# Kernel tuning notes

Measured on AMD Instinct MI355X. Metric: run time of the kernel, lower is better.

Reference implementation:

```python
import jax, jax.numpy as jnp
import numpy as np

B, T, C = 4, 4096, 1024
NH, DH = 16, 128          # n_head, d_head = d_qkv // n_head
DQKV, DR = 2048, 256      # d_qkv, d_rank


def _uniform(key, shape, bound):
    return jax.random.uniform(key, shape, jnp.float32, -bound, bound)


def setup_inputs() -> dict:
    key = jax.random.key(0)
    k0, k1, k2, k3, k4 = jax.random.split(key, 5)
    # CastedLinear init: bound = sqrt(3) * 0.5 * in_features**-0.5 (same for w1, w2)
    b_qkv = (3 ** 0.5) * 0.5 * C ** (-0.5)
    b_proj = (3 ** 0.5) * 0.5 * DQKV ** (-0.5)
    return {
        "x": jax.random.normal(k0, (B, T, C), jnp.float32),
        "qkv_w1": _uniform(k1, (DR, C), b_qkv),
        "qkv_w2": _uniform(k2, (3 * DQKV, DR), b_qkv),
        "cproj_w1": _uniform(k3, (DR, DQKV), b_proj),
        "cproj_w2": _uniform(k4, (2 * C, DR), b_proj),
    }


def _rmsnorm(x):
    eps = jnp.finfo(x.dtype).eps  # F.rms_norm default eps
    return x * jax.lax.rsqrt(jnp.mean(x * x, axis=-1, keepdims=True) + eps)


def reference(x, qkv_w1, qkv_w2, cproj_w1, cproj_w2):
    Bx, Tx, Cx = x.shape
    # qkv projection with low-rank factorization + relu^2 activation between factors
    h = _rmsnorm(x) @ qkv_w1.T                      # [B,T,DR]
    h = jnp.square(jax.nn.relu(h))
    qkv = (h @ qkv_w2.T).reshape(Bx, Tx, 3 * NH, DH)
    q, k, v = jnp.split(qkv, 3, axis=2)             # each [B,T,NH,DH]
    q, k = _rmsnorm(q), _rmsnorm(k)

    # rotary embedding: half the head dim rotated, second quarter frequencies zero
    quarter = DH // 4
    freq = (1.0 / 1024.0) ** jnp.linspace(0.0, 1.0, quarter)
    freq = jnp.concatenate([freq, jnp.zeros(quarter, freq.dtype)])  # [DH//2]
    theta = jnp.arange(Tx, dtype=jnp.float32)[:, None] * freq[None, :]
    cos = jnp.cos(theta)[None, :, None, :]          # [1,T,1,DH//2]
    sin = jnp.sin(theta)[None, :, None, :]

    def rope(z):
        z1, z2 = jnp.split(z, 2, axis=-1)
        return jnp.concatenate([z1 * cos + z2 * sin, -z1 * sin + z2 * cos], axis=-1)

    q, k = rope(q), rope(k)

    # causal linear attention: sigmoid-gated cumulative sum over time
    y = jax.nn.relu(q) * jnp.cumsum(jax.nn.sigmoid(k) * v, axis=1)  # [B,T,NH,DH]
    y = y.reshape(Bx, Tx, NH * DH)

    # low-rank output projection (no activation), gated residual
    uv = (y @ cproj_w1.T) @ cproj_w2.T              # [B,T,2C]
    u, g = jnp.split(uv, 2, axis=-1)
    return x + u * jax.nn.silu(g)
```

## Files before the change

kernel.cpp:

```cpp
#include <hip/hip_runtime.h>
#include <hip/hip_bf16.h>

#define TB 4
#define TT 4096
#define TC 1024
#define TNH 16
#define TDH 128
#define TDQKV 2048
#define TDR 256
#define RB 4096
#define ROWS (TB*TT)
#define SLAB (RB*128)

typedef __attribute__((ext_vector_type(8))) short bfx8;
typedef __attribute__((ext_vector_type(4))) float fx4;
typedef __attribute__((address_space(1))) const unsigned char GAS;
typedef __attribute__((address_space(3))) unsigned char LAS;

__device__ __forceinline__ unsigned short f2b(float f) {
    unsigned int u = __float_as_uint(f);
    unsigned int r = (u + 0x7fffu + ((u >> 16) & 1u)) >> 16;
    return (unsigned short)r;
}
__device__ __forceinline__ float b2f(unsigned short h) {
    return __uint_as_float(((unsigned int)h) << 16);
}
__device__ __forceinline__ float sigm(float x) {
    return 1.0f / (1.0f + __expf(-x));
}
__device__ __forceinline__ int xcd_swz(int hw, int nwg) {
    int q = nwg >> 3;
    return (hw & 7) * q + (hw >> 3);
}

__global__ __launch_bounds__(256) void cvt_bf16(const float* __restrict__ in,
                                                unsigned short* __restrict__ out, int n) {
    int i = (blockIdx.x * 256 + threadIdx.x) * 4;
    if (i < n) {
        float4 v = *(const float4*)(in + i);
        out[i + 0] = f2b(v.x);
        out[i + 1] = f2b(v.y);
        out[i + 2] = f2b(v.z);
        out[i + 3] = f2b(v.w);
    }
}

__global__ __launch_bounds__(256) void rope_tab(float* __restrict__ ct, float* __restrict__ st) {
    int i = blockIdx.x * 256 + threadIdx.x;
    int t = i >> 5, j = i & 31;
    float fr = exp2f(-10.0f * (float)j / 31.0f);
    float th = (float)t * fr;
    ct[i] = cosf(th);
    st[i] = sinf(th);
}

__global__ __launch_bounds__(256) void rmsnorm_x(const float* __restrict__ x,
                                                 unsigned short* __restrict__ xn) {
    int row = blockIdx.x;
    int tid = threadIdx.x;
    float4 v = *(const float4*)(x + (size_t)row * TC + tid * 4);
    float ss = v.x * v.x + v.y * v.y + v.z * v.z + v.w * v.w;
    #pragma unroll
    for (int o = 32; o > 0; o >>= 1) ss += __shfl_xor(ss, o);
    __shared__ float red[4];
    if ((tid & 63) == 0) red[tid >> 6] = ss;
    __syncthreads();
    float tot = red[0] + red[1] + red[2] + red[3];
    float sc = rsqrtf(tot * (1.0f / TC) + 1.1920929e-7f);
    unsigned short* o = xn + (size_t)row * TC + tid * 4;
    o[0] = f2b(v.x * sc); o[1] = f2b(v.y * sc); o[2] = f2b(v.z * sc); o[3] = f2b(v.w * sc);
}

template <int EPI>
__global__ __launch_bounds__(256) void gemm_bt(const unsigned short* __restrict__ A, int lda,
                                               const unsigned short* __restrict__ Bm,
                                               unsigned short* __restrict__ C, int ldc,
                                               int N, int K) {
    __shared__ unsigned short As[2][128 * 32];
    __shared__ unsigned short Bs[2][128 * 32];
    const int m0 = blockIdx.y * 128;
    const int n0 = blockIdx.x * 128;
    const int tid = threadIdx.x;
    const int lane = tid & 63;
    const int w = tid >> 6;
    const int wr = w >> 1, wc = w & 1;
    const int r16 = lane & 15;
    const int kk = (lane >> 4) * 8;
    const int l4 = lane >> 2;
    const int c8 = (lane & 3) * 8;
    const int nk = K >> 5;
    fx4 acc[4][4] = {};

    auto stage = [&](int buf, int k0) {
        #pragma unroll
        for (int i = 0; i < 2; ++i) {
            int rr = (w + 4 * i) * 16 + l4;
            const unsigned short* ga = A + (size_t)(m0 + rr) * lda + k0 + c8;
            const unsigned short* gb = Bm + (size_t)(n0 + rr) * K + k0 + c8;
            __builtin_amdgcn_global_load_lds((GAS*)ga, (LAS*)&As[buf][(w + 4 * i) * 512], 16, 0, 0);
            __builtin_amdgcn_global_load_lds((GAS*)gb, (LAS*)&Bs[buf][(w + 4 * i) * 512], 16, 0, 0);
        }
    };

    stage(0, 0);
    __syncthreads();
    int buf = 0;
    for (int ks = 0; ks < nk; ++ks) {
        if (ks + 1 < nk) stage(buf ^ 1, (ks + 1) * 32);
        bfx8 af[4], bfr[4];
        #pragma unroll
        for (int mi = 0; mi < 4; mi++) af[mi] = *(const bfx8*)&As[buf][(wr * 64 + mi * 16 + r16) * 32 + kk];
        #pragma unroll
        for (int ni = 0; ni < 4; ni++) bfr[ni] = *(const bfx8*)&Bs[buf][(wc * 64 + ni * 16 + r16) * 32 + kk];
        #pragma unroll
        for (int mi = 0; mi < 4; mi++)
            #pragma unroll
            for (int ni = 0; ni < 4; ni++)
                acc[mi][ni] = __builtin_amdgcn_mfma_f32_16x16x32_bf16(af[mi], bfr[ni], acc[mi][ni], 0, 0, 0);
        __syncthreads();
        buf ^= 1;
    }

    const int rg = lane >> 4;
    #pragma unroll
    for (int mi = 0; mi < 4; mi++)
        #pragma unroll
        for (int ni = 0; ni < 4; ni++) {
            int col = n0 + wc * 64 + ni * 16 + r16;
            #pragma unroll
            for (int r = 0; r < 4; r++) {
                int row = m0 + wr * 64 + mi * 16 + rg * 4 + r;
                float v = acc[mi][ni][r];
                if (EPI == 1) { v = fmaxf(v, 0.0f); v *= v; }
                if (EPI == 2) {
                    int head = col >> 7;
                    C[(size_t)head * SLAB + (size_t)row * 128 + (col & 127)] = f2b(v);
                } else {
                    C[(size_t)row * ldc + col] = f2b(v);
                }
            }
        }
}

template <int EPI, int NX>
__global__ __launch_bounds__(256) void gemm_bt64(const unsigned short* __restrict__ A, int lda,
                                                 const unsigned short* __restrict__ Bm,
                                                 unsigned short* __restrict__ C, int ldc,
                                                 int K) {
    __shared__ unsigned short As[2][64 * 32];
    __shared__ unsigned short Bs[2][64 * 32];
    const int hw = blockIdx.y * gridDim.x + blockIdx.x;
    const int lg = xcd_swz(hw, gridDim.x * gridDim.y);
    const int n0 = (lg % NX) * 64;
    const int m0 = (lg / NX) * 64;
    const int tid = threadIdx.x;
    const int lane = tid & 63;
    const int w = tid >> 6;
    const int wr = w >> 1, wc = w & 1;
    const int r16 = lane & 15;
    const int kk = (lane >> 4) * 8;
    const int l4 = lane >> 2;
    const int c8 = (lane & 3) * 8;
    const int nk = K >> 5;
    fx4 acc[2][2] = {};

    auto stage = [&](int buf, int k0) {
        int rr = w * 16 + l4;
        const unsigned short* ga = A + (size_t)(m0 + rr) * lda + k0 + c8;
        const unsigned short* gb = Bm + (size_t)(n0 + rr) * K + k0 + c8;
        __builtin_amdgcn_global_load_lds((GAS*)ga, (LAS*)&As[buf][w * 512], 16, 0, 0);
        __builtin_amdgcn_global_load_lds((GAS*)gb, (LAS*)&Bs[buf][w * 512], 16, 0, 0);
    };

    stage(0, 0);
    __syncthreads();
    int buf = 0;
    for (int ks = 0; ks < nk; ++ks) {
        if (ks + 1 < nk) stage(buf ^ 1, (ks + 1) * 32);
        bfx8 af[2], bfr[2];
        #pragma unroll
        for (int mi = 0; mi < 2; mi++) af[mi] = *(const bfx8*)&As[buf][(wr * 32 + mi * 16 + r16) * 32 + kk];
        #pragma unroll
        for (int ni = 0; ni < 2; ni++) bfr[ni] = *(const bfx8*)&Bs[buf][(wc * 32 + ni * 16 + r16) * 32 + kk];
        #pragma unroll
        for (int mi = 0; mi < 2; mi++)
            #pragma unroll
            for (int ni = 0; ni < 2; ni++)
                acc[mi][ni] = __builtin_amdgcn_mfma_f32_16x16x32_bf16(af[mi], bfr[ni], acc[mi][ni], 0, 0, 0);
        __syncthreads();
        buf ^= 1;
    }

    const int rg = lane >> 4;
    #pragma unroll
    for (int mi = 0; mi < 2; mi++)
        #pragma unroll
        for (int ni = 0; ni < 2; ni++) {
            int col = n0 + wc * 32 + ni * 16 + r16;
            #pragma unroll
            for (int r = 0; r < 4; r++) {
                int row = m0 + wr * 32 + mi * 16 + rg * 4 + r;
                float v = acc[mi][ni][r];
                if (EPI == 1) { v = fmaxf(v, 0.0f); v *= v; }
                C[(size_t)row * ldc + col] = f2b(v);
            }
        }
}

__global__ __launch_bounds__(256, 2) void gemm4f(const unsigned short* __restrict__ A,
                                                 const unsigned short* __restrict__ Wm,
                                                 const float* __restrict__ x,
                                                 float* __restrict__ out) {
    __shared__ unsigned short As[2][128 * 32];
    __shared__ unsigned short Bu[2][128 * 32];
    __shared__ unsigned short Bg[2][128 * 32];
    const int hw = blockIdx.y * gridDim.x + blockIdx.x;
    const int lg = xcd_swz(hw, gridDim.x * gridDim.y);
    const int n0 = (lg & 7) * 128;
    const int m0 = (lg >> 3) * 128;
    const int tid = threadIdx.x;
    const int lane = tid & 63;
    const int w = tid >> 6;
    const int wr = w >> 1, wc = w & 1;
    const int r16 = lane & 15;
    const int kk = (lane >> 4) * 8;
    const int l4 = lane >> 2;
    const int c8 = (lane & 3) * 8;
    fx4 accu[4][4] = {};
    fx4 accg[4][4] = {};

    auto stage = [&](int buf, int k0) {
        #pragma unroll
        for (int i = 0; i < 2; ++i) {
            int rr = (w + 4 * i) * 16 + l4;
            const unsigned short* ga = A + (size_t)(m0 + rr) * TDR + k0 + c8;
            const unsigned short* gu = Wm + (size_t)(n0 + rr) * TDR + k0 + c8;
            const unsigned short* gg = Wm + (size_t)(1024 + n0 + rr) * TDR + k0 + c8;
            __builtin_amdgcn_global_load_lds((GAS*)ga, (LAS*)&As[buf][(w + 4 * i) * 512], 16, 0, 0);
            __builtin_amdgcn_global_load_lds((GAS*)gu, (LAS*)&Bu[buf][(w + 4 * i) * 512], 16, 0, 0);
            __builtin_amdgcn_global_load_lds((GAS*)gg, (LAS*)&Bg[buf][(w + 4 * i) * 512], 16, 0, 0);
        }
    };

    stage(0, 0);
    __syncthreads();
    int buf = 0;
    for (int ks = 0; ks < 8; ++ks) {
        if (ks + 1 < 8) stage(buf ^ 1, (ks + 1) * 32);
        bfx8 af[4], bu[4], bg[4];
        #pragma unroll
        for (int mi = 0; mi < 4; mi++) af[mi] = *(const bfx8*)&As[buf][(wr * 64 + mi * 16 + r16) * 32 + kk];
        #pragma unroll
        for (int ni = 0; ni < 4; ni++) {
            bu[ni] = *(const bfx8*)&Bu[buf][(wc * 64 + ni * 16 + r16) * 32 + kk];
            bg[ni] = *(const bfx8*)&Bg[buf][(wc * 64 + ni * 16 + r16) * 32 + kk];
        }
        #pragma unroll
        for (int mi = 0; mi < 4; mi++)
            #pragma unroll
            for (int ni = 0; ni < 4; ni++) {
                accu[mi][ni] = __builtin_amdgcn_mfma_f32_16x16x32_bf16(af[mi], bu[ni], accu[mi][ni], 0, 0, 0);
                accg[mi][ni] = __builtin_amdgcn_mfma_f32_16x16x32_bf16(af[mi], bg[ni], accg[mi][ni], 0, 0, 0);
            }
        __syncthreads();
        buf ^= 1;
    }

    const int rg = lane >> 4;
    #pragma unroll
    for (int mi = 0; mi < 4; mi++)
        #pragma unroll
        for (int ni = 0; ni < 4; ni++) {
            int col = n0 + wc * 64 + ni * 16 + r16;
            #pragma unroll
            for (int r = 0; r < 4; r++) {
                int row = m0 + wr * 64 + mi * 16 + rg * 4 + r;
                float u = accu[mi][ni][r];
                float g = accg[mi][ni][r];
                size_t idx = (size_t)row * TC + col;
                out[idx] = x[idx] + u * (g * sigm(g));
            }
        }
}

__global__ __launch_bounds__(256) void qk_post(unsigned short* __restrict__ qkv,
                                               const float* __restrict__ ct,
                                               const float* __restrict__ st) {
    int gri = blockIdx.x * 4 + (threadIdx.x >> 6);
    int lane = threadIdx.x & 63;
    int h32 = gri >> 12;
    int t = gri & (RB - 1);
    size_t base = (size_t)h32 * SLAB + (size_t)t * 128;
    float e0 = b2f(qkv[base + lane]);
    float e1 = b2f(qkv[base + 64 + lane]);
    float ss = e0 * e0 + e1 * e1;
    #pragma unroll
    for (int o = 32; o > 0; o >>= 1) ss += __shfl_xor(ss, o);
    float sc = rsqrtf(ss * (1.0f / TDH) + 1.1920929e-7f);
    float z1 = e0 * sc, z2 = e1 * sc, o1, o2;
    if (lane < 32) {
        float c = ct[t * 32 + lane], s = st[t * 32 + lane];
        o1 = z1 * c + z2 * s;
        o2 = z2 * c - z1 * s;
    } else {
        o1 = z1; o2 = z2;
    }
    qkv[base + lane] = f2b(o1);
    qkv[base + 64 + lane] = f2b(o2);
}

__global__ __launch_bounds__(128) void scanA(const unsigned short* __restrict__ qkv,
                                             float* __restrict__ part) {
    int blk = blockIdx.x;
    int d = threadIdx.x;
    int s = blk & 63;
    int h = blk >> 6;
    const unsigned short* kp = qkv + (size_t)(16 + h) * SLAB + (size_t)(s * 64) * 128 + d;
    const unsigned short* vp = qkv + (size_t)(32 + h) * SLAB + (size_t)(s * 64) * 128 + d;
    float sum = 0.0f;
    #pragma unroll 8
    for (int t = 0; t < 64; ++t) {
        float kv = b2f(kp[t * 128]);
        float vv = b2f(vp[t * 128]);
        sum += sigm(kv) * vv;
    }
    part[(size_t)blk * 128 + d] = sum;
}

__global__ __launch_bounds__(256) void scanB(float* __restrict__ part) {
    int idx = blockIdx.x * 256 + threadIdx.x;
    int h = idx >> 7, d = idx & 127;
    float v[64];
    #pragma unroll
    for (int s = 0; s < 64; ++s) v[s] = part[((size_t)(h * 64 + s)) * 128 + d];
    float run = 0.0f;
    #pragma unroll
    for (int s = 0; s < 64; ++s) { float tv = v[s]; v[s] = run; run += tv; }
    #pragma unroll
    for (int s = 0; s < 64; ++s) part[((size_t)(h * 64 + s)) * 128 + d] = v[s];
}

__global__ __launch_bounds__(128) void scanC(const unsigned short* __restrict__ qkv,
                                             const float* __restrict__ part,
                                             unsigned short* __restrict__ y) {
    int blk = blockIdx.x;
    int d = threadIdx.x;
    int s = blk & 63;
    int h = blk >> 6;
    const unsigned short* qp = qkv + (size_t)h * SLAB + (size_t)(s * 64) * 128 + d;
    const unsigned short* kp = qkv + (size_t)(16 + h) * SLAB + (size_t)(s * 64) * 128 + d;
    const unsigned short* vp = qkv + (size_t)(32 + h) * SLAB + (size_t)(s * 64) * 128 + d;
    float sum = part[(size_t)blk * 128 + d];
    size_t yb = (size_t)(s * 64) * 2048 + (size_t)h * 128 + d;
    #pragma unroll 4
    for (int t = 0; t < 64; ++t) {
        float kv = b2f(kp[t * 128]);
        float vv = b2f(vp[t * 128]);
        sum += sigm(kv) * vv;
        float qv = b2f(qp[t * 128]);
        y[yb + (size_t)t * 2048] = f2b(fmaxf(qv, 0.0f) * sum);
    }
}

extern "C" void kernel_launch(void* const* d_in, const int* in_sizes, int n_in,
                              void* d_out, int out_size, void* d_ws, size_t ws_size,
                              hipStream_t stream) {
    (void)in_sizes; (void)n_in; (void)out_size; (void)ws_size;
    const float* x    = (const float*)d_in[0];
    const float* wq1  = (const float*)d_in[1];
    const float* wq2  = (const float*)d_in[2];
    const float* wc1  = (const float*)d_in[3];
    const float* wc2  = (const float*)d_in[4];
    float* out = (float*)d_out;

    char* ws = (char*)d_ws;
    size_t off = 0;
    auto alloc = [&](size_t bytes) -> void* {
        off = (off + 255) & ~(size_t)255;
        void* p = ws + off;
        off += bytes;
        return p;
    };
    char* pool = (char*)alloc((size_t)RB * 6144 * 2);
    unsigned short* qkvb = (unsigned short*)pool;
    unsigned short* xn   = (unsigned short*)pool;
    unsigned short* t1   = (unsigned short*)pool;
    unsigned short* hbuf = (unsigned short*)alloc((size_t)ROWS * TDR * 2);
    unsigned short* w1b  = (unsigned short*)alloc((size_t)TDR * TC * 2);
    unsigned short* w2b  = (unsigned short*)alloc((size_t)3 * TDQKV * TDR * 2);
    unsigned short* wp1b = (unsigned short*)alloc((size_t)TDR * TDQKV * 2);
    unsigned short* wp2b = (unsigned short*)alloc((size_t)2 * TC * TDR * 2);
    float* ct   = (float*)alloc((size_t)TT * 32 * 4);
    float* st   = (float*)alloc((size_t)TT * 32 * 4);
    float* part = (float*)alloc((size_t)TNH * 64 * 128 * 4);
    unsigned short* ybuf = (unsigned short*)d_out;

    cvt_bf16<<<(TDR * TC) / 1024, 256, 0, stream>>>(wq1, w1b, TDR * TC);
    cvt_bf16<<<(3 * TDQKV * TDR) / 1024, 256, 0, stream>>>(wq2, w2b, 3 * TDQKV * TDR);
    cvt_bf16<<<(TDR * TDQKV) / 1024, 256, 0, stream>>>(wc1, wp1b, TDR * TDQKV);
    cvt_bf16<<<(2 * TC * TDR) / 1024, 256, 0, stream>>>(wc2, wp2b, 2 * TC * TDR);
    rope_tab<<<(TT * 32) / 256, 256, 0, stream>>>(ct, st);

    rmsnorm_x<<<ROWS, 256, 0, stream>>>(x, xn);
    gemm_bt64<1, 4><<<dim3(TDR / 64, ROWS / 64), 256, 0, stream>>>(
        xn, TC, w1b, hbuf, TDR, TC);

    for (int b = 0; b < TB; ++b) {
        gemm_bt<2><<<dim3(6144 / 128, RB / 128), 256, 0, stream>>>(
            hbuf + (size_t)b * RB * TDR, TDR, w2b, qkvb, 0, 6144, TDR);
        qk_post<<<(RB * 32) / 4, 256, 0, stream>>>(qkvb, ct, st);
        scanA<<<TNH * 64, 128, 0, stream>>>(qkvb, part);
        scanB<<<(TNH * 128) / 256, 256, 0, stream>>>(part);
        scanC<<<TNH * 64, 128, 0, stream>>>(qkvb, part, ybuf + (size_t)b * RB * 2048);
    }

    gemm_bt64<0, 4><<<dim3(TDR / 64, ROWS / 64), 256, 0, stream>>>(
        ybuf, 2048, wp1b, t1, TDR, TDQKV);
    gemm4f<<<dim3(TC / 128, ROWS / 128), 256, 0, stream>>>(t1, wp2b, x, out);
}
```

Before: 412.4 us.

## Fuse qk norm/rope with scan partial sums and shrink final GEMM tile

Merges the q/k RMSnorm+rope pass with the first scan pass: one kernel normalizes q and k, applies rope, computes sigmoid(k)*v, writes rotated q and the gated product back into the k slab, and emits per-segment partial sums. The final scan then reads only q and the precomputed product instead of k and v, so it does less traffic and skips the sigmoid. Separately, the fused output GEMM moves from 128x128 to 64x64 tiles, which gives more blocks and fewer registers per thread but less data reuse per tile. Storing the product in bf16 before accumulation changes rounding slightly.

```diff
diff --git a/kernel.cpp b/kernel.cpp
--- a/kernel.cpp
+++ b/kernel.cpp
@@ -207,17 +207,17 @@
         }
 }
 
-__global__ __launch_bounds__(256, 2) void gemm4f(const unsigned short* __restrict__ A,
-                                                 const unsigned short* __restrict__ Wm,
-                                                 const float* __restrict__ x,
-                                                 float* __restrict__ out) {
-    __shared__ unsigned short As[2][128 * 32];
-    __shared__ unsigned short Bu[2][128 * 32];
-    __shared__ unsigned short Bg[2][128 * 32];
+__global__ __launch_bounds__(256) void gemm4f64(const unsigned short* __restrict__ A,
+                                                const unsigned short* __restrict__ Wm,
+                                                const float* __restrict__ x,
+                                                float* __restrict__ out) {
+    __shared__ unsigned short As[2][64 * 32];
+    __shared__ unsigned short Bu[2][64 * 32];
+    __shared__ unsigned short Bg[2][64 * 32];
     const int hw = blockIdx.y * gridDim.x + blockIdx.x;
     const int lg = xcd_swz(hw, gridDim.x * gridDim.y);
-    const int n0 = (lg & 7) * 128;
-    const int m0 = (lg >> 3) * 128;
+    const int n0 = (lg & 15) * 64;
+    const int m0 = (lg >> 4) * 64;
     const int tid = threadIdx.x;
     const int lane = tid & 63;
     const int w = tid >> 6;
@@ -226,20 +226,17 @@
     const int kk = (lane >> 4) * 8;
     const int l4 = lane >> 2;
     const int c8 = (lane & 3) * 8;
-    fx4 accu[4][4] = {};
-    fx4 accg[4][4] = {};
+    fx4 accu[2][2] = {};
+    fx4 accg[2][2] = {};
 
     auto stage = [&](int buf, int k0) {
-        #pragma unroll
-        for (int i = 0; i < 2; ++i) {
-            int rr = (w + 4 * i) * 16 + l4;
-            const unsigned short* ga = A + (size_t)(m0 + rr) * TDR + k0 + c8;
-            const unsigned short* gu = Wm + (size_t)(n0 + rr) * TDR + k0 + c8;
-            const unsigned short* gg = Wm + (size_t)(1024 + n0 + rr) * TDR + k0 + c8;
-            __builtin_amdgcn_global_load_lds((GAS*)ga, (LAS*)&As[buf][(w + 4 * i) * 512], 16, 0, 0);
-            __builtin_amdgcn_global_load_lds((GAS*)gu, (LAS*)&Bu[buf][(w + 4 * i) * 512], 16, 0, 0);
-            __builtin_amdgcn_global_load_lds((GAS*)gg, (LAS*)&Bg[buf][(w + 4 * i) * 512], 16, 0, 0);
-        }
+        int rr = w * 16 + l4;
+        const unsigned short* ga = A + (size_t)(m0 + rr) * TDR + k0 + c8;
+        const unsigned short* gu = Wm + (size_t)(n0 + rr) * TDR + k0 + c8;
+        const unsigned short* gg = Wm + (size_t)(1024 + n0 + rr) * TDR + k0 + c8;
+        __builtin_amdgcn_global_load_lds((GAS*)ga, (LAS*)&As[buf][w * 512], 16, 0, 0);
+        __builtin_amdgcn_global_load_lds((GAS*)gu, (LAS*)&Bu[buf][w * 512], 16, 0, 0);
+        __builtin_amdgcn_global_load_lds((GAS*)gg, (LAS*)&Bg[buf][w * 512], 16, 0, 0);
     };
 
     stage(0, 0);
@@ -247,18 +244,18 @@
     int buf = 0;
     for (int ks = 0; ks < 8; ++ks) {
         if (ks + 1 < 8) stage(buf ^ 1, (ks + 1) * 32);
-        bfx8 af[4], bu[4], bg[4];
-        #pragma unroll
-        for (int mi = 0; mi < 4; mi++) af[mi] = *(const bfx8*)&As[buf][(wr * 64 + mi * 16 + r16) * 32 + kk];
-        #pragma unroll
-        for (int ni = 0; ni < 4; ni++) {
-            bu[ni] = *(const bfx8*)&Bu[buf][(wc * 64 + ni * 16 + r16) * 32 + kk];
-            bg[ni] = *(const bfx8*)&Bg[buf][(wc * 64 + ni * 16 + r16) * 32 + kk];
-        }
-        #pragma unroll
-        for (int mi = 0; mi < 4; mi++)
-            #pragma unroll
-            for (int ni = 0; ni < 4; ni++) {
+        bfx8 af[2], bu[2], bg[2];
+        #pragma unroll
+        for (int mi = 0; mi < 2; mi++) af[mi] = *(const bfx8*)&As[buf][(wr * 32 + mi * 16 + r16) * 32 + kk];
+        #pragma unroll
+        for (int ni = 0; ni < 2; ni++) {
+            bu[ni] = *(const bfx8*)&Bu[buf][(wc * 32 + ni * 16 + r16) * 32 + kk];
+            bg[ni] = *(const bfx8*)&Bg[buf][(wc * 32 + ni * 16 + r16) * 32 + kk];
+        }
+        #pragma unroll
+        for (int mi = 0; mi < 2; mi++)
+            #pragma unroll
+            for (int ni = 0; ni < 2; ni++) {
                 accu[mi][ni] = __builtin_amdgcn_mfma_f32_16x16x32_bf16(af[mi], bu[ni], accu[mi][ni], 0, 0, 0);
                 accg[mi][ni] = __builtin_amdgcn_mfma_f32_16x16x32_bf16(af[mi], bg[ni], accg[mi][ni], 0, 0, 0);
             }
@@ -268,13 +265,13 @@
 
     const int rg = lane >> 4;
     #pragma unroll
-    for (int mi = 0; mi < 4; mi++)
-        #pragma unroll
-        for (int ni = 0; ni < 4; ni++) {
-            int col = n0 + wc * 64 + ni * 16 + r16;
+    for (int mi = 0; mi < 2; mi++)
+        #pragma unroll
+        for (int ni = 0; ni < 2; ni++) {
+            int col = n0 + wc * 32 + ni * 16 + r16;
             #pragma unroll
             for (int r = 0; r < 4; r++) {
-                int row = m0 + wr * 64 + mi * 16 + rg * 4 + r;
+                int row = m0 + wr * 32 + mi * 16 + rg * 4 + r;
                 float u = accu[mi][ni][r];
                 float g = accg[mi][ni][r];
                 size_t idx = (size_t)row * TC + col;
@@ -283,48 +280,70 @@
         }
 }
 
-__global__ __launch_bounds__(256) void qk_post(unsigned short* __restrict__ qkv,
+__global__ __launch_bounds__(256) void post128(unsigned short* __restrict__ qkv,
                                                const float* __restrict__ ct,
-                                               const float* __restrict__ st) {
-    int gri = blockIdx.x * 4 + (threadIdx.x >> 6);
-    int lane = threadIdx.x & 63;
-    int h32 = gri >> 12;
-    int t = gri & (RB - 1);
-    size_t base = (size_t)h32 * SLAB + (size_t)t * 128;
-    float e0 = b2f(qkv[base + lane]);
-    float e1 = b2f(qkv[base + 64 + lane]);
-    float ss = e0 * e0 + e1 * e1;
-    #pragma unroll
-    for (int o = 32; o > 0; o >>= 1) ss += __shfl_xor(ss, o);
-    float sc = rsqrtf(ss * (1.0f / TDH) + 1.1920929e-7f);
-    float z1 = e0 * sc, z2 = e1 * sc, o1, o2;
-    if (lane < 32) {
-        float c = ct[t * 32 + lane], s = st[t * 32 + lane];
-        o1 = z1 * c + z2 * s;
-        o2 = z2 * c - z1 * s;
-    } else {
-        o1 = z1; o2 = z2;
-    }
-    qkv[base + lane] = f2b(o1);
-    qkv[base + 64 + lane] = f2b(o2);
-}
-
-__global__ __launch_bounds__(128) void scanA(const unsigned short* __restrict__ qkv,
-                                             float* __restrict__ part) {
-    int blk = blockIdx.x;
-    int d = threadIdx.x;
-    int s = blk & 63;
-    int h = blk >> 6;
-    const unsigned short* kp = qkv + (size_t)(16 + h) * SLAB + (size_t)(s * 64) * 128 + d;
-    const unsigned short* vp = qkv + (size_t)(32 + h) * SLAB + (size_t)(s * 64) * 128 + d;
-    float sum = 0.0f;
-    #pragma unroll 8
-    for (int t = 0; t < 64; ++t) {
-        float kv = b2f(kp[t * 128]);
-        float vv = b2f(vp[t * 128]);
-        sum += sigm(kv) * vv;
-    }
-    part[(size_t)blk * 128 + d] = sum;
+                                               const float* __restrict__ st,
+                                               float* __restrict__ part) {
+    const int blk = blockIdx.x;
+    const int mb = blk & 31, h = blk >> 5;
+    const int w = threadIdx.x >> 6, lane = threadIdx.x & 63;
+    unsigned short* qs = qkv + (size_t)h * SLAB;
+    unsigned short* ks = qkv + (size_t)(16 + h) * SLAB;
+    unsigned short* vs = qkv + (size_t)(32 + h) * SLAB;
+    __shared__ float psum[4][2][128];
+    const int d0 = lane * 2;
+    const float sgn = (lane < 32) ? 1.0f : -1.0f;
+    const int jh = lane & 31;
+
+    #pragma unroll
+    for (int half = 0; half < 2; ++half) {
+        float a0 = 0.0f, a1 = 0.0f;
+        for (int i = half * 16; i < half * 16 + 16; ++i) {
+            int r = i * 4 + w;
+            int t = mb * 128 + r;
+            size_t off = (size_t)t * 128 + d0;
+            ushort2 q2 = *(const ushort2*)(qs + off);
+            ushort2 k2 = *(const ushort2*)(ks + off);
+            float q0 = b2f(q2.x), q1 = b2f(q2.y);
+            float k0 = b2f(k2.x), k1 = b2f(k2.y);
+            float ssq = q0 * q0 + q1 * q1;
+            float ssk = k0 * k0 + k1 * k1;
+            #pragma unroll
+            for (int o = 32; o > 0; o >>= 1) {
+                ssq += __shfl_xor(ssq, o);
+                ssk += __shfl_xor(ssk, o);
+            }
+            float qsc = rsqrtf(ssq * (1.0f / TDH) + 1.1920929e-7f);
+            float ksc = rsqrtf(ssk * (1.0f / TDH) + 1.1920929e-7f);
+            q0 *= qsc; q1 *= qsc; k0 *= ksc; k1 *= ksc;
+            float qp0 = __shfl_xor(q0, 32), qp1 = __shfl_xor(q1, 32);
+            float kp0 = __shfl_xor(k0, 32), kp1 = __shfl_xor(k1, 32);
+            float c0 = 1.0f, c1 = 1.0f, s0 = 0.0f, s1 = 0.0f;
+            if (jh < 16) {
+                const float* cb = ct + t * 32 + jh * 2;
+                const float* sb = st + t * 32 + jh * 2;
+                c0 = cb[0]; c1 = cb[1]; s0 = sb[0] * sgn; s1 = sb[1] * sgn;
+            }
+            float qo0 = q0 * c0 + qp0 * s0;
+            float qo1 = q1 * c1 + qp1 * s1;
+            float ko0 = k0 * c0 + kp0 * s0;
+            float ko1 = k1 * c1 + kp1 * s1;
+            ushort2 v2 = *(const ushort2*)(vs + off);
+            float p0 = sigm(ko0) * b2f(v2.x);
+            float p1 = sigm(ko1) * b2f(v2.y);
+            ushort2 qo; qo.x = f2b(qo0); qo.y = f2b(qo1);
+            ushort2 po; po.x = f2b(p0);  po.y = f2b(p1);
+            *(ushort2*)(qs + off) = qo;
+            *(ushort2*)(ks + off) = po;
+            a0 += p0; a1 += p1;
+        }
+        psum[w][half][d0] = a0;
+        psum[w][half][d0 + 1] = a1;
+    }
+    __syncthreads();
+    int seg = threadIdx.x >> 7, d = threadIdx.x & 127;
+    float tot = psum[0][seg][d] + psum[1][seg][d] + psum[2][seg][d] + psum[3][seg][d];
+    part[(size_t)(h * 64 + mb * 2 + seg) * 128 + d] = tot;
 }
 
 __global__ __launch_bounds__(256) void scanB(float* __restrict__ part) {
@@ -340,23 +359,20 @@
     for (int s = 0; s < 64; ++s) part[((size_t)(h * 64 + s)) * 128 + d] = v[s];
 }
 
-__global__ __launch_bounds__(128) void scanC(const unsigned short* __restrict__ qkv,
-                                             const float* __restrict__ part,
-                                             unsigned short* __restrict__ y) {
+__global__ __launch_bounds__(128) void scanC2(const unsigned short* __restrict__ qkv,
+                                              const float* __restrict__ part,
+                                              unsigned short* __restrict__ y) {
     int blk = blockIdx.x;
     int d = threadIdx.x;
     int s = blk & 63;
     int h = blk >> 6;
     const unsigned short* qp = qkv + (size_t)h * SLAB + (size_t)(s * 64) * 128 + d;
-    const unsigned short* kp = qkv + (size_t)(16 + h) * SLAB + (size_t)(s * 64) * 128 + d;
-    const unsigned short* vp = qkv + (size_t)(32 + h) * SLAB + (size_t)(s * 64) * 128 + d;
+    const unsigned short* pp = qkv + (size_t)(16 + h) * SLAB + (size_t)(s * 64) * 128 + d;
     float sum = part[(size_t)blk * 128 + d];
     size_t yb = (size_t)(s * 64) * 2048 + (size_t)h * 128 + d;
     #pragma unroll 4
     for (int t = 0; t < 64; ++t) {
-        float kv = b2f(kp[t * 128]);
-        float vv = b2f(vp[t * 128]);
-        sum += sigm(kv) * vv;
+        sum += b2f(pp[t * 128]);
         float qv = b2f(qp[t * 128]);
         y[yb + (size_t)t * 2048] = f2b(fmaxf(qv, 0.0f) * sum);
     }
@@ -408,13 +424,12 @@
     for (int b = 0; b < TB; ++b) {
         gemm_bt<2><<<dim3(6144 / 128, RB / 128), 256, 0, stream>>>(
             hbuf + (size_t)b * RB * TDR, TDR, w2b, qkvb, 0, 6144, TDR);
-        qk_post<<<(RB * 32) / 4, 256, 0, stream>>>(qkvb, ct, st);
-        scanA<<<TNH * 64, 128, 0, stream>>>(qkvb, part);
+        post128<<<TNH * 32, 256, 0, stream>>>(qkvb, ct, st, part);
         scanB<<<(TNH * 128) / 256, 256, 0, stream>>>(part);
-        scanC<<<TNH * 64, 128, 0, stream>>>(qkvb, part, ybuf + (size_t)b * RB * 2048);
+        scanC2<<<TNH * 64, 128, 0, stream>>>(qkvb, part, ybuf + (size_t)b * RB * 2048);
     }
 
     gemm_bt64<0, 4><<<dim3(TDR / 64, ROWS / 64), 256, 0, stream>>>(
         ybuf, 2048, wp1b, t1, TDR, TDQKV);
-    gemm4f<<<dim3(TC / 128, ROWS / 128), 256, 0, stream>>>(t1, wp2b, x, out);
-}
+    gemm4f64<<<dim3(TC / 64, ROWS / 64), 256, 0, stream>>>(t1, wp2b, x, out);
+}
```

After: 425.3 us. 3.1% more time.
